# Kernel tuning notes

Measured on AMD Instinct MI355X. Metric: run time of the kernel, lower is better.

## Reference

```python
import jax, jax.numpy as jnp
import numpy as np

N_NODES = 100000


def _gcn_conv(x, src, dst, w_edge, W, b, n_nodes):
    # PyG GCNConv: deg computed at target (col) with self-loop weights included
    deg = jax.ops.segment_sum(w_edge, dst, num_segments=n_nodes)
    dinv = jnp.where(deg > 0, jax.lax.rsqrt(deg), 0.0)
    norm = dinv[src] * w_edge * dinv[dst]            # [E+N]
    h = x @ W                                        # [N, out] linear (no bias yet)
    msg = norm[:, None] * h[src]                     # gather + scale, [E+N, out]
    out = jax.ops.segment_sum(msg, dst, num_segments=n_nodes)  # scatter-add at target
    return out + b


def setup_inputs() -> dict:
    key = jax.random.key(0)
    k1, k2, k3, k4, k5 = jax.random.split(key, 5)
    n, din, dh, dout = N_NODES, 128, 128, 64
    E = 1600000
    x = jax.random.normal(k1, (n, din), dtype=jnp.float32)
    edge_index = jax.random.randint(k2, (2, E), 0, n, dtype=jnp.int64)
    # Glorot-ish init for layer weights, zero bias (PyG default)
    W1 = jax.random.normal(k3, (din, dh), dtype=jnp.float32) / np.sqrt(din)
    b1 = jnp.zeros((dh,), dtype=jnp.float32)
    W2 = jax.random.normal(k4, (dh, dout), dtype=jnp.float32) / np.sqrt(dh)
    b2 = jnp.zeros((dout,), dtype=jnp.float32)
    return {"x": x, "edge_index": edge_index, "W1": W1, "b1": b1, "W2": W2, "b2": b2}


def reference(x, edge_index, W1, b1, W2, b2):
    n = x.shape[0]
    # add self-loops with weight 1 (PyG add_self_loops + fill_value=1)
    loop = jnp.arange(n, dtype=edge_index.dtype)
    src = jnp.concatenate([edge_index[0], loop])
    dst = jnp.concatenate([edge_index[1], loop])
    w_edge = jnp.ones(src.shape[0], dtype=x.dtype)

    h = _gcn_conv(x, src, dst, w_edge, W1, b1, n)
    h = jax.nn.relu(h)
    # dropout: eval mode (identity)
    out = _gcn_conv(h, src, dst, w_edge, W2, b2, n)
    return out
```

## Files before the change

### kernel.cpp

```cpp
#include <hip/hip_runtime.h>

typedef _Float16 half2v __attribute__((ext_vector_type(2)));
typedef _Float16 half4v __attribute__((ext_vector_type(4)));
typedef _Float16 f16x8 __attribute__((ext_vector_type(8)));
typedef float f32x4 __attribute__((ext_vector_type(4)));

#define NBKT_MAX 256
#define BKT_CAP  16384
#define OVF_CAP  8192

__global__ void wcast_kernel(const float* __restrict__ W, _Float16* __restrict__ Wt) {
    int t = blockIdx.x * 256 + threadIdx.x;
    if (t < 128 * 128) {
        int k = t >> 7, c = t & 127;
        Wt[c * 128 + k] = (_Float16)W[k * 128 + c];
    }
}

__global__ void scan1_kernel(const int* __restrict__ deg, int* __restrict__ rowstart,
                             int* __restrict__ blockSums, float* __restrict__ dinv, int n) {
    __shared__ int tmp[256];
    int t = threadIdx.x;
    int i = blockIdx.x * 256 + t;
    int v = (i < n) ? deg[i] : 0;
    if (i < n) dinv[i] = rsqrtf((float)(v + 1));
    tmp[t] = v;
    __syncthreads();
#pragma unroll
    for (int off = 1; off < 256; off <<= 1) {
        int add = (t >= off) ? tmp[t - off] : 0;
        __syncthreads();
        tmp[t] += add;
        __syncthreads();
    }
    if (i < n) rowstart[i] = tmp[t] - v;
    if (t == 255) blockSums[blockIdx.x] = tmp[255];
}

__global__ void scan2_kernel(int* __restrict__ blockSums, int nb) {
    __shared__ int tmp[512];
    int t = threadIdx.x;
    int v = (t < nb) ? blockSums[t] : 0;
    tmp[t] = v;
    __syncthreads();
#pragma unroll
    for (int off = 1; off < 512; off <<= 1) {
        int add = (t >= off) ? tmp[t - off] : 0;
        __syncthreads();
        tmp[t] += add;
        __syncthreads();
    }
    if (t < nb) blockSums[t] = tmp[t] - v;
}

__global__ void scan3_kernel(int* __restrict__ rowstart, const int* __restrict__ blockSums, int n) {
    int i = blockIdx.x * blockDim.x + threadIdx.x;
    if (i < n) rowstart[i] += blockSums[i >> 8];
}

__global__ __launch_bounds__(256) void scale_h1_kernel(_Float16* __restrict__ h1,
                                                       const float* __restrict__ dinv, int n) {
    int j = blockIdx.x * 256 + threadIdx.x;
    if (j < n * 16) {
        float dv = dinv[j >> 4];
        f16x8 v = ((const f16x8*)h1)[j];
#pragma unroll
        for (int k = 0; k < 8; k++) v[k] = (_Float16)((float)v[k] * dv);
        ((f16x8*)h1)[j] = v;
    }
}

__global__ __launch_bounds__(256) void part_gemm1_kernel(
        const int* __restrict__ src, const int* __restrict__ dst,
        int* __restrict__ deg, int* __restrict__ bktCnt, int* __restrict__ ovfCnt,
        int2* __restrict__ ovfBuf, int2* __restrict__ pairPart, int E,
        const float* __restrict__ x, const _Float16* __restrict__ Wt,
        _Float16* __restrict__ h, int n, int nbkt) {
    __shared__ union {
        _Float16 xs_h[64][128];
        struct { int cnt[NBKT_MAX]; int gbase[NBKT_MAX]; int off[NBKT_MAX]; } s;
    } u;
    int bid = blockIdx.x;
    int t = threadIdx.x;
    if (bid % 3 != 2) {
        int gb = (bid / 3) * 2 + (bid % 3);
        int node0 = gb * 64;
        if (node0 >= n) return;

#pragma unroll
        for (int i = 0; i < 4; i++) {
            int fi = t + 256 * i;
            int row = fi >> 4, seg = fi & 15;
            float4 a = make_float4(0.f, 0.f, 0.f, 0.f);
            float4 b4 = make_float4(0.f, 0.f, 0.f, 0.f);
            if (node0 + row < n) {
                const float4* xr = (const float4*)(x + (size_t)(node0 + row) * 128 + seg * 8);
                a = xr[0]; b4 = xr[1];
            }
            f16x8 hv;
            hv[0] = (_Float16)a.x;  hv[1] = (_Float16)a.y;
            hv[2] = (_Float16)a.z;  hv[3] = (_Float16)a.w;
            hv[4] = (_Float16)b4.x; hv[5] = (_Float16)b4.y;
            hv[6] = (_Float16)b4.z; hv[7] = (_Float16)b4.w;
            int byte = row * 256 + ((seg * 16) ^ ((row & 7) << 4));
            *(f16x8*)((char*)&u.xs_h[0][0] + byte) = hv;
        }
        __syncthreads();

        int wid = t >> 6, l = t & 63;
        int row0 = wid * 16;
        int arow = row0 + (l & 15);
        int kgrp = l >> 4;
        f32x4 acc[8];
#pragma unroll
        for (int ct = 0; ct < 8; ct++) acc[ct] = (f32x4){0.f, 0.f, 0.f, 0.f};

        const char* xbase = (const char*)&u.xs_h[0][0] + arow * 256;
#pragma unroll
        for (int ks = 0; ks < 4; ks++) {
            int abyte = ((ks * 64 + kgrp * 16) ^ ((arow & 7) << 4));
            f16x8 afrag = *(const f16x8*)(xbase + abyte);
#pragma unroll
            for (int ct = 0; ct < 8; ct++) {
                f16x8 bfrag = *(const f16x8*)(Wt + (ct * 16 + (l & 15)) * 128 + ks * 32 + kgrp * 8);
                acc[ct] = __builtin_amdgcn_mfma_f32_16x16x32_f16(afrag, bfrag, acc[ct], 0, 0, 0);
            }
        }

        int r0 = row0 + kgrp * 4;
#pragma unroll
        for (int ct = 0; ct < 8; ct++) {
            int col = ct * 16 + (l & 15);
#pragma unroll
            for (int r = 0; r < 4; r++) {
                int node = node0 + r0 + r;
                if (node < n)
                    h[(size_t)node * 128 + col] = (_Float16)acc[ct][r];
            }
        }
    } else {
        int sb = bid / 3;
        int base = sb * 2048;
        if (base >= E) return;
        for (int i = t; i < nbkt; i += 256) u.s.cnt[i] = 0;
        __syncthreads();
        int s_[8], d_[8];
#pragma unroll
        for (int j = 0; j < 8; j++) {
            int e = base + t + 256 * j;
            s_[j] = -1;
            if (e < E) {
                s_[j] = src[e];
                d_[j] = dst[e];
                atomicAdd(&deg[d_[j]], 1);
                atomicAdd(&u.s.cnt[d_[j] >> 9], 1);
            }
        }
        __syncthreads();
        for (int i = t; i < nbkt; i += 256) {
            u.s.off[i] = 0;
            int c = u.s.cnt[i];
            if (c > 0) u.s.gbase[i] = atomicAdd(&bktCnt[i], c);
        }
        __syncthreads();
#pragma unroll
        for (int j = 0; j < 8; j++) {
            if (s_[j] >= 0) {
                int b = d_[j] >> 9;
                int slot = u.s.gbase[b] + atomicAdd(&u.s.off[b], 1);
                if (slot < BKT_CAP) {
                    pairPart[(size_t)b * BKT_CAP + slot] = make_int2(s_[j], d_[j]);
                } else {
                    int op = atomicAdd(ovfCnt, 1);
                    if (op < OVF_CAP) ovfBuf[op] = make_int2(s_[j], d_[j]);
                }
            }
        }
    }
}

__global__ __launch_bounds__(256) void scatter2_kernel(
        const int2* __restrict__ pairPart, const int* __restrict__ bktCnt,
        const int* __restrict__ ovfCnt, const int2* __restrict__ ovfBuf,
        const int* __restrict__ rowstart,
        int* __restrict__ srcSorted, int n) {
    __shared__ int lcur[512];
    int b = blockIdx.x;
    int t = threadIdx.x;
    int node0 = b << 9;
#pragma unroll
    for (int i = 0; i < 2; i++) {
        int node = node0 + t + 256 * i;
        if (node < n) lcur[t + 256 * i] = rowstart[node];
    }
    __syncthreads();
    int cnt = bktCnt[b];
    if (cnt > BKT_CAP) cnt = BKT_CAP;
    const int2* bp = pairPart + (size_t)b * BKT_CAP;
    for (int e = t; e < cnt; e += 256) {
        int2 p = bp[e];
        int pos = atomicAdd(&lcur[p.y - node0], 1);
        srcSorted[pos] = p.x;
    }
    int oc = *ovfCnt;
    if (oc > 0) {
        if (oc > OVF_CAP) oc = OVF_CAP;
        for (int i = t; i < oc; i += 256) {
            int2 p = ovfBuf[i];
            if ((p.y >> 9) == b) {
                int pos = atomicAdd(&lcur[p.y - node0], 1);
                srcSorted[pos] = p.x;
            }
        }
    }
}

__global__ __launch_bounds__(256) void gather1_kernel(
        const int* __restrict__ srcS, const int* __restrict__ rowstart,
        const int* __restrict__ deg, const float* __restrict__ dinv,
        const _Float16* __restrict__ h1, const float* __restrict__ b1,
        float* __restrict__ h2, int n) {
    int t = threadIdx.x;
    int g = __builtin_amdgcn_readfirstlane(blockIdx.x * 4 + (t >> 6));
    int lane = t & 63;
    if (g >= n) return;

    float dg = dinv[g];
    half2v sv0 = ((const half2v*)(h1 + (size_t)g * 128))[lane];
    float2 acc = make_float2((float)sv0.x, (float)sv0.y);
    int beg = rowstart[g], end = beg + deg[g];
    int e = beg;
    while (e < end) {
        int rem = end - e;
        int sv = (lane < rem) ? srcS[e + lane] : 0;
        int chunk = rem < 64 ? rem : 64;
        int j = 0;
        for (; j + 8 <= chunk; j += 8) {
            int s0 = __shfl(sv, j + 0), s1 = __shfl(sv, j + 1);
            int s2 = __shfl(sv, j + 2), s3 = __shfl(sv, j + 3);
            int s4 = __shfl(sv, j + 4), s5 = __shfl(sv, j + 5);
            int s6 = __shfl(sv, j + 6), s7 = __shfl(sv, j + 7);
            half2v u0 = ((const half2v*)(h1 + (size_t)s0 * 128))[lane];
            half2v u1 = ((const half2v*)(h1 + (size_t)s1 * 128))[lane];
            half2v u2 = ((const half2v*)(h1 + (size_t)s2 * 128))[lane];
            half2v u3 = ((const half2v*)(h1 + (size_t)s3 * 128))[lane];
            half2v u4 = ((const half2v*)(h1 + (size_t)s4 * 128))[lane];
            half2v u5 = ((const half2v*)(h1 + (size_t)s5 * 128))[lane];
            half2v u6 = ((const half2v*)(h1 + (size_t)s6 * 128))[lane];
            half2v u7 = ((const half2v*)(h1 + (size_t)s7 * 128))[lane];
            acc.x += (float)u0.x; acc.y += (float)u0.y;
            acc.x += (float)u1.x; acc.y += (float)u1.y;
            acc.x += (float)u2.x; acc.y += (float)u2.y;
            acc.x += (float)u3.x; acc.y += (float)u3.y;
            acc.x += (float)u4.x; acc.y += (float)u4.y;
            acc.x += (float)u5.x; acc.y += (float)u5.y;
            acc.x += (float)u6.x; acc.y += (float)u6.y;
            acc.x += (float)u7.x; acc.y += (float)u7.y;
        }
        for (; j < chunk; j++) {
            int s = __shfl(sv, j);
            half2v u = ((const half2v*)(h1 + (size_t)s * 128))[lane];
            acc.x += (float)u.x; acc.y += (float)u.y;
        }
        e += chunk;
    }
    float2 b = ((const float2*)b1)[lane];
    acc.x = fmaxf(dg * acc.x + b.x, 0.f);
    acc.y = fmaxf(dg * acc.y + b.y, 0.f);
    ((float2*)(h2 + (size_t)g * 128))[lane] = acc;
}

__global__ __launch_bounds__(256) void gemm_nk64(const float* __restrict__ x,
                                                 const float* __restrict__ W,
                                                 const float* __restrict__ dinv,
                                                 _Float16* __restrict__ h, int n) {
    __shared__ float xs[32][128];
    int t = threadIdx.x;
    int node0 = blockIdx.x * 32;
#pragma unroll
    for (int i = 0; i < 4; i++) {
        int fi = t + 256 * i;
        int row = fi >> 5, cv = fi & 31;
        float4 v = make_float4(0.f, 0.f, 0.f, 0.f);
        if (node0 + row < n) v = ((const float4*)x)[(size_t)(node0 + row) * 32 + cv];
        ((float4*)(&xs[0][0]))[fi] = v;
    }
    __syncthreads();

    int tx = t & 15, ty = t >> 4;
    int c0 = tx * 4;
    float acc[2][4];
#pragma unroll
    for (int i = 0; i < 2; i++)
#pragma unroll
        for (int j = 0; j < 4; j++) acc[i][j] = 0.f;

    for (int k = 0; k < 128; k++) {
        float4 w = *(const float4*)(W + k * 64 + c0);
#pragma unroll
        for (int i = 0; i < 2; i++) {
            float xval = xs[ty + 16 * i][k];
            acc[i][0] += xval * w.x;
            acc[i][1] += xval * w.y;
            acc[i][2] += xval * w.z;
            acc[i][3] += xval * w.w;
        }
    }
#pragma unroll
    for (int i = 0; i < 2; i++) {
        int node = node0 + ty + 16 * i;
        if (node < n) {
            float dv = dinv[node];
            half4v hv;
            hv.x = (_Float16)(acc[i][0] * dv);
            hv.y = (_Float16)(acc[i][1] * dv);
            hv.z = (_Float16)(acc[i][2] * dv);
            hv.w = (_Float16)(acc[i][3] * dv);
            *(half4v*)(h + (size_t)node * 64 + c0) = hv;
        }
    }
}

__global__ __launch_bounds__(256) void gather2_kernel(
        const int* __restrict__ srcS, const int* __restrict__ rowstart,
        const int* __restrict__ deg, const float* __restrict__ dinv,
        const _Float16* __restrict__ h3, const float* __restrict__ b2,
        float* __restrict__ out, int n) {
    int t = threadIdx.x;
    int g = __builtin_amdgcn_readfirstlane(blockIdx.x * 4 + (t >> 6));
    int lane = t & 63;
    if (g >= n) return;
    float dg = dinv[g];
    float acc = (float)h3[(size_t)g * 64 + lane];
    int beg = rowstart[g], end = beg + deg[g];
    int e = beg;
    while (e < end) {
        int rem = end - e;
        int sv = (lane < rem) ? srcS[e + lane] : 0;
        int chunk = rem < 64 ? rem : 64;
        int j = 0;
        for (; j + 8 <= chunk; j += 8) {
            int s0 = __shfl(sv, j + 0), s1 = __shfl(sv, j + 1);
            int s2 = __shfl(sv, j + 2), s3 = __shfl(sv, j + 3);
            int s4 = __shfl(sv, j + 4), s5 = __shfl(sv, j + 5);
            int s6 = __shfl(sv, j + 6), s7 = __shfl(sv, j + 7);
            float u0 = (float)h3[(size_t)s0 * 64 + lane];
            float u1 = (float)h3[(size_t)s1 * 64 + lane];
            float u2 = (float)h3[(size_t)s2 * 64 + lane];
            float u3 = (float)h3[(size_t)s3 * 64 + lane];
            float u4 = (float)h3[(size_t)s4 * 64 + lane];
            float u5 = (float)h3[(size_t)s5 * 64 + lane];
            float u6 = (float)h3[(size_t)s6 * 64 + lane];
            float u7 = (float)h3[(size_t)s7 * 64 + lane];
            acc += u0 + u1 + u2 + u3 + u4 + u5 + u6 + u7;
        }
        for (; j < chunk; j++) {
            int s = __shfl(sv, j);
            acc += (float)h3[(size_t)s * 64 + lane];
        }
        e += chunk;
    }
    out[(size_t)g * 64 + lane] = dg * acc + b2[lane];
}

extern "C" void kernel_launch(void* const* d_in, const int* in_sizes, int n_in,
                              void* d_out, int out_size, void* d_ws, size_t ws_size,
                              hipStream_t stream) {
    const float* x  = (const float*)d_in[0];
    const int*   ei = (const int*)d_in[1];
    const float* W1 = (const float*)d_in[2];
    const float* b1 = (const float*)d_in[3];
    const float* W2 = (const float*)d_in[4];
    const float* b2 = (const float*)d_in[5];
    float* out = (float*)d_out;

    const int n = in_sizes[0] / 128;
    const int E = in_sizes[1] / 2;
    const int* src = ei;
    const int* dst = ei + E;
    const int nb = (n + 255) / 256;
    const int nbkt = (n + 511) >> 9;

    char* ws = (char*)d_ws;
    size_t off = 0;
    auto carve = [&](size_t bytes) -> char* {
        char* p = ws + off;
        off += (bytes + 255) & ~(size_t)255;
        return p;
    };
    int*   deg       = (int*)carve((size_t)n * 4);
    int*   bktCnt    = (int*)carve((size_t)NBKT_MAX * 4);
    int*   ovfCnt    = (int*)carve(4);
    size_t msz       = (size_t)((char*)ovfCnt - (char*)deg) + 256;
    float* dinv      = (float*)carve((size_t)n * 4);
    int*   rowstart  = (int*)carve((size_t)n * 4);
    int*   blockSums = (int*)carve((size_t)nb * 4);
    int*   srcSorted = (int*)carve((size_t)E * 4);
    _Float16* Wt     = (_Float16*)carve((size_t)128 * 128 * 2);
    int2*  ovfBuf    = (int2*)carve((size_t)OVF_CAP * 8);
    _Float16* h1     = (_Float16*)carve((size_t)n * 128 * 2);
    float* bufB      = (float*)carve((size_t)n * 128 * 4);
    int2*  pairPart  = (int2*)bufB;
    _Float16* h3     = h1;

    hipMemsetAsync(deg, 0, msz, stream);

    wcast_kernel<<<64, 256, 0, stream>>>(W1, Wt);

    int sortBlocks = (E + 2047) / 2048;
    int gemmBlocks = (n + 63) / 64;
    int triples = sortBlocks;
    int gtr = (gemmBlocks + 1) / 2;
    if (gtr > triples) triples = gtr;
    int G = triples * 3;
    part_gemm1_kernel<<<G, 256, 0, stream>>>(src, dst, deg, bktCnt, ovfCnt, ovfBuf,
                                             pairPart, E, x, Wt, h1, n, nbkt);

    scan1_kernel<<<nb, 256, 0, stream>>>(deg, rowstart, blockSums, dinv, n);
    scan2_kernel<<<1, 512, 0, stream>>>(blockSums, nb);
    scan3_kernel<<<(n + 255) / 256, 256, 0, stream>>>(rowstart, blockSums, n);

    scale_h1_kernel<<<(n * 16 + 255) / 256, 256, 0, stream>>>(h1, dinv, n);

    scatter2_kernel<<<nbkt, 256, 0, stream>>>(pairPart, bktCnt, ovfCnt, ovfBuf,
                                              rowstart, srcSorted, n);

    gather1_kernel<<<(n + 3) / 4, 256, 0, stream>>>(srcSorted, rowstart, deg, dinv,
                                                    h1, b1, bufB, n);

    gemm_nk64<<<(n + 31) / 32, 256, 0, stream>>>(bufB, W2, dinv, h3, n);
    gather2_kernel<<<(n + 3) / 4, 256, 0, stream>>>(srcSorted, rowstart, deg, dinv,
                                                    h3, b2, out, n);
}
```

Measured before the change: 386.7 us.

## Pack edge pairs into 32 bits and compute degrees per bucket in shared memory

Edge pairs in the bucket buffer are packed into one 32-bit word (local dst offset in the high bits, src in the low 17 bits), halving partition traffic. Global atomic degree counting is removed from the partition pass and replaced by a new per-bucket kernel that builds a shared-memory histogram. Partition blocks now handle 8192 edges each with an 8:1 gemm-to-partition interleave. The scan3 and h1 scaling kernels are fused into one launch. This adds an extra pass over the bucket data, and the packing assumes node ids fit in 17 bits.

```diff
diff --git a/kernel.cpp b/kernel.cpp
--- a/kernel.cpp
+++ b/kernel.cpp
@@ -8,6 +8,7 @@
 #define NBKT_MAX 256
 #define BKT_CAP  16384
 #define OVF_CAP  8192
+#define SRC_MASK 0x1FFFF
 
 __global__ void wcast_kernel(const float* __restrict__ W, _Float16* __restrict__ Wt) {
     int t = blockIdx.x * 256 + threadIdx.x;
@@ -53,14 +54,11 @@
     if (t < nb) blockSums[t] = tmp[t] - v;
 }
 
-__global__ void scan3_kernel(int* __restrict__ rowstart, const int* __restrict__ blockSums, int n) {
-    int i = blockIdx.x * blockDim.x + threadIdx.x;
-    if (i < n) rowstart[i] += blockSums[i >> 8];
-}
-
-__global__ __launch_bounds__(256) void scale_h1_kernel(_Float16* __restrict__ h1,
-                                                       const float* __restrict__ dinv, int n) {
+__global__ __launch_bounds__(256) void scan3_scale_kernel(
+        int* __restrict__ rowstart, const int* __restrict__ blockSums,
+        _Float16* __restrict__ h1, const float* __restrict__ dinv, int n) {
     int j = blockIdx.x * 256 + threadIdx.x;
+    if (j < n) rowstart[j] += blockSums[j >> 8];
     if (j < n * 16) {
         float dv = dinv[j >> 4];
         f16x8 v = ((const f16x8*)h1)[j];
@@ -72,8 +70,8 @@
 
 __global__ __launch_bounds__(256) void part_gemm1_kernel(
         const int* __restrict__ src, const int* __restrict__ dst,
-        int* __restrict__ deg, int* __restrict__ bktCnt, int* __restrict__ ovfCnt,
-        int2* __restrict__ ovfBuf, int2* __restrict__ pairPart, int E,
+        int* __restrict__ bktCnt, int* __restrict__ ovfCnt,
+        int2* __restrict__ ovfBuf, unsigned* __restrict__ pairPart, int E,
         const float* __restrict__ x, const _Float16* __restrict__ Wt,
         _Float16* __restrict__ h, int n, int nbkt) {
     __shared__ union {
@@ -82,8 +80,8 @@
     } u;
     int bid = blockIdx.x;
     int t = threadIdx.x;
-    if (bid % 3 != 2) {
-        int gb = (bid / 3) * 2 + (bid % 3);
+    if (bid % 9 != 8) {
+        int gb = (bid / 9) * 8 + (bid % 9);
         int node0 = gb * 64;
         if (node0 >= n) return;
 
@@ -139,23 +137,14 @@
             }
         }
     } else {
-        int sb = bid / 3;
-        int base = sb * 2048;
+        int sb = bid / 9;
+        int base = sb * 8192;
         if (base >= E) return;
+        int eend = base + 8192; if (eend > E) eend = E;
         for (int i = t; i < nbkt; i += 256) u.s.cnt[i] = 0;
         __syncthreads();
-        int s_[8], d_[8];
-#pragma unroll
-        for (int j = 0; j < 8; j++) {
-            int e = base + t + 256 * j;
-            s_[j] = -1;
-            if (e < E) {
-                s_[j] = src[e];
-                d_[j] = dst[e];
-                atomicAdd(&deg[d_[j]], 1);
-                atomicAdd(&u.s.cnt[d_[j] >> 9], 1);
-            }
-        }
+        for (int e = base + t; e < eend; e += 256)
+            atomicAdd(&u.s.cnt[dst[e] >> 9], 1);
         __syncthreads();
         for (int i = t; i < nbkt; i += 256) {
             u.s.off[i] = 0;
@@ -163,24 +152,51 @@
             if (c > 0) u.s.gbase[i] = atomicAdd(&bktCnt[i], c);
         }
         __syncthreads();
-#pragma unroll
-        for (int j = 0; j < 8; j++) {
-            if (s_[j] >= 0) {
-                int b = d_[j] >> 9;
-                int slot = u.s.gbase[b] + atomicAdd(&u.s.off[b], 1);
-                if (slot < BKT_CAP) {
-                    pairPart[(size_t)b * BKT_CAP + slot] = make_int2(s_[j], d_[j]);
-                } else {
-                    int op = atomicAdd(ovfCnt, 1);
-                    if (op < OVF_CAP) ovfBuf[op] = make_int2(s_[j], d_[j]);
-                }
+        for (int e = base + t; e < eend; e += 256) {
+            int s = src[e], d = dst[e];
+            int b = d >> 9;
+            int slot = u.s.gbase[b] + atomicAdd(&u.s.off[b], 1);
+            unsigned p = ((unsigned)(d & 511) << 17) | (unsigned)s;
+            if (slot < BKT_CAP) {
+                pairPart[(size_t)b * BKT_CAP + slot] = p;
+            } else {
+                int op = atomicAdd(ovfCnt, 1);
+                if (op < OVF_CAP) ovfBuf[op] = make_int2((int)p, b);
             }
         }
     }
 }
 
+__global__ __launch_bounds__(256) void deg_bucket_kernel(
+        const unsigned* __restrict__ pairPart, const int* __restrict__ bktCnt,
+        const int* __restrict__ ovfCnt, const int2* __restrict__ ovfBuf,
+        int* __restrict__ deg, int n) {
+    __shared__ int hist[512];
+    int b = blockIdx.x;
+    int t = threadIdx.x;
+    hist[t] = 0; hist[t + 256] = 0;
+    __syncthreads();
+    int cnt = bktCnt[b];
+    if (cnt > BKT_CAP) cnt = BKT_CAP;
+    const unsigned* bp = pairPart + (size_t)b * BKT_CAP;
+    for (int e = t; e < cnt; e += 256)
+        atomicAdd(&hist[bp[e] >> 17], 1);
+    int oc = *ovfCnt;
+    if (oc > 0) {
+        if (oc > OVF_CAP) oc = OVF_CAP;
+        for (int i = t; i < oc; i += 256) {
+            int2 p = ovfBuf[i];
+            if (p.y == b) atomicAdd(&hist[((unsigned)p.x) >> 17], 1);
+        }
+    }
+    __syncthreads();
+    int node0 = b << 9;
+    if (node0 + t < n)       deg[node0 + t]       = hist[t];
+    if (node0 + t + 256 < n) deg[node0 + t + 256] = hist[t + 256];
+}
+
 __global__ __launch_bounds__(256) void scatter2_kernel(
-        const int2* __restrict__ pairPart, const int* __restrict__ bktCnt,
+        const unsigned* __restrict__ pairPart, const int* __restrict__ bktCnt,
         const int* __restrict__ ovfCnt, const int2* __restrict__ ovfBuf,
         const int* __restrict__ rowstart,
         int* __restrict__ srcSorted, int n) {
@@ -196,20 +212,20 @@
     __syncthreads();
     int cnt = bktCnt[b];
     if (cnt > BKT_CAP) cnt = BKT_CAP;
-    const int2* bp = pairPart + (size_t)b * BKT_CAP;
+    const unsigned* bp = pairPart + (size_t)b * BKT_CAP;
     for (int e = t; e < cnt; e += 256) {
-        int2 p = bp[e];
-        int pos = atomicAdd(&lcur[p.y - node0], 1);
-        srcSorted[pos] = p.x;
+        unsigned p = bp[e];
+        int pos = atomicAdd(&lcur[p >> 17], 1);
+        srcSorted[pos] = (int)(p & SRC_MASK);
     }
     int oc = *ovfCnt;
     if (oc > 0) {
         if (oc > OVF_CAP) oc = OVF_CAP;
         for (int i = t; i < oc; i += 256) {
             int2 p = ovfBuf[i];
-            if ((p.y >> 9) == b) {
-                int pos = atomicAdd(&lcur[p.y - node0], 1);
-                srcSorted[pos] = p.x;
+            if (p.y == b) {
+                int pos = atomicAdd(&lcur[((unsigned)p.x) >> 17], 1);
+                srcSorted[pos] = (int)((unsigned)p.x & SRC_MASK);
             }
         }
     }
@@ -388,10 +404,10 @@
         off += (bytes + 255) & ~(size_t)255;
         return p;
     };
-    int*   deg       = (int*)carve((size_t)n * 4);
     int*   bktCnt    = (int*)carve((size_t)NBKT_MAX * 4);
     int*   ovfCnt    = (int*)carve(4);
-    size_t msz       = (size_t)((char*)ovfCnt - (char*)deg) + 256;
+    size_t msz       = (size_t)((char*)ovfCnt - (char*)bktCnt) + 256;
+    int*   deg       = (int*)carve((size_t)n * 4);
     float* dinv      = (float*)carve((size_t)n * 4);
     int*   rowstart  = (int*)carve((size_t)n * 4);
     int*   blockSums = (int*)carve((size_t)nb * 4);
@@ -400,27 +416,26 @@
     int2*  ovfBuf    = (int2*)carve((size_t)OVF_CAP * 8);
     _Float16* h1     = (_Float16*)carve((size_t)n * 128 * 2);
     float* bufB      = (float*)carve((size_t)n * 128 * 4);
-    int2*  pairPart  = (int2*)bufB;
+    unsigned* pairPart = (unsigned*)bufB;
     _Float16* h3     = h1;
 
-    hipMemsetAsync(deg, 0, msz, stream);
+    hipMemsetAsync(bktCnt, 0, msz, stream);
 
     wcast_kernel<<<64, 256, 0, stream>>>(W1, Wt);
 
-    int sortBlocks = (E + 2047) / 2048;
+    int sortBlocks = (E + 8191) / 8192;
     int gemmBlocks = (n + 63) / 64;
-    int triples = sortBlocks;
-    int gtr = (gemmBlocks + 1) / 2;
-    if (gtr > triples) triples = gtr;
-    int G = triples * 3;
-    part_gemm1_kernel<<<G, 256, 0, stream>>>(src, dst, deg, bktCnt, ovfCnt, ovfBuf,
+    int gGroups = (gemmBlocks + 7) / 8;
+    int groups = (sortBlocks > gGroups) ? sortBlocks : gGroups;
+    int G = groups * 9;
+    part_gemm1_kernel<<<G, 256, 0, stream>>>(src, dst, bktCnt, ovfCnt, ovfBuf,
                                              pairPart, E, x, Wt, h1, n, nbkt);
+
+    deg_bucket_kernel<<<nbkt, 256, 0, stream>>>(pairPart, bktCnt, ovfCnt, ovfBuf, deg, n);
 
     scan1_kernel<<<nb, 256, 0, stream>>>(deg, rowstart, blockSums, dinv, n);
     scan2_kernel<<<1, 512, 0, stream>>>(blockSums, nb);
-    scan3_kernel<<<(n + 255) / 256, 256, 0, stream>>>(rowstart, blockSums, n);
-
-    scale_h1_kernel<<<(n * 16 + 255) / 256, 256, 0, stream>>>(h1, dinv, n);
+    scan3_scale_kernel<<<(n * 16 + 255) / 256, 256, 0, stream>>>(rowstart, blockSums, h1, dinv, n);
 
     scatter2_kernel<<<nbkt, 256, 0, stream>>>(pairPart, bktCnt, ovfCnt, ovfBuf,
                                               rowstart, srcSorted, n);
```

Measured after the change: 368.6 us. 1.05x faster.
